# Kernel tuning notes

Measured on AMD Instinct MI355X. Metric: run time of the kernel, lower is better.

The kernel has to match this reference:

```python
import jax, jax.numpy as jnp
import numpy as np

COMMITMENT_COST = 0.25
EPS = 1e-10


def setup_inputs() -> dict:
    key = jax.random.key(0)
    k1, k2 = jax.random.split(key)
    z = jax.random.normal(k1, (8, 2048, 512), dtype=jnp.float32)
    # codebook ~ small uniform init in torch; small normal is fine for a numeric reference
    codebook = jax.random.normal(k2, (4096, 512), dtype=jnp.float32) * 0.02
    return {"z": z, "codebook": codebook}


def reference(z, codebook):
    B, S, D = z.shape
    K = codebook.shape[0]
    flat_z = z.reshape(-1, D)  # [N, D]
    distances = (
        jnp.sum(flat_z * flat_z, axis=1, keepdims=True)
        + jnp.sum(codebook * codebook, axis=1)
        - 2.0 * flat_z @ codebook.T
    )
    encoding_indices = jnp.argmin(distances, axis=1)  # [N] int
    z_q = codebook[encoding_indices].reshape(z.shape)  # gather lookup
    # commitment loss (z_q detached)
    commitment_loss = jnp.mean((z - jax.lax.stop_gradient(z_q)) ** 2)
    loss = COMMITMENT_COST * commitment_loss
    # straight-through estimator
    z_q_st = z + jax.lax.stop_gradient(z_q - z)
    # perplexity from codebook usage histogram
    N = flat_z.shape[0]
    counts = jnp.zeros((K,), dtype=jnp.float32).at[encoding_indices].add(1.0)
    avg_probs = counts / N
    perplexity = jnp.exp(-jnp.sum(avg_probs * jnp.log(avg_probs + EPS)))
    encoding_indices = encoding_indices.reshape(B, S)
    return (z_q_st, loss, encoding_indices, perplexity)
```

## Files before the change

kernel.cpp:

```cpp
#include <hip/hip_runtime.h>
#include <hip/hip_fp16.h>
#include <stdint.h>

#define B_  8
#define S_  2048
#define D_  512
#define K_  4096
#define N_  (B_ * S_)
#define NCB (K_ / 128)
#define NKB (D_ / 32)
#define MARGIN 4e-3f

typedef _Float16 half8  __attribute__((ext_vector_type(8)));
typedef float    floatx4 __attribute__((ext_vector_type(4)));

#define OFF_PV0  0
#define OFF_PI0  (OFF_PV0 + (size_t)N_ * NCB * 4)
#define OFF_PV1  (OFF_PI0 + (size_t)N_ * NCB * 4)
#define OFF_PI1  (OFF_PV1 + (size_t)N_ * NCB * 4)
#define OFF_EN   (OFF_PI1 + (size_t)N_ * NCB * 4)
#define OFF_ZN   (OFF_EN + K_ * 4)
#define OFF_CNT  (OFF_ZN + N_ * 4)
#define OFF_BL   (OFF_CNT + K_ * 4)
#define OFF_ZH   (OFF_BL + 4096 * 4)
#define OFF_EH   (OFF_ZH + (size_t)N_ * D_ * 2)

__device__ __forceinline__ bool lexlt(float va, int ia, float vb, int ib) {
    return va < vb || (va == vb && ia < ib);
}

__device__ __forceinline__ void load_lds16(const _Float16* g, _Float16* l) {
    __builtin_amdgcn_global_load_lds(
        (const __attribute__((address_space(1))) unsigned int*)(uintptr_t)g,
        (__attribute__((address_space(3))) unsigned int*)(uintptr_t)l,
        16, 0, 0);
}

__global__ __launch_bounds__(256)
void vq_prep_kernel(const float* __restrict__ z, const float* __restrict__ cb,
                    _Float16* __restrict__ zh, _Float16* __restrict__ eh,
                    float* __restrict__ znorm, float* __restrict__ enorm,
                    int* __restrict__ counts) {
    const int t = threadIdx.x;
    if (blockIdx.x < 16) counts[blockIdx.x * 256 + t] = 0;

    const size_t u = (size_t)blockIdx.x * 256 + t;
    const int c   = (int)(u & 63);
    const int row = (int)(u >> 6);
    const bool isZ = row < N_;
    const int n = isZ ? row : row - N_;
    const float* r = (isZ ? z : cb) + (size_t)n * D_;

    float s = 0.f;
    for (int j = c; j < D_; j += 64) { float v = r[j]; s += v * v; }
    #pragma unroll
    for (int m = 1; m < 64; m <<= 1) s += __shfl_xor(s, m, 64);
    if (c == 0) { if (isZ) znorm[n] = s; else enorm[n] = s; }

    const float scale = isZ ? 1.0f : 64.0f;
    const float4 v0 = *(const float4*)(r + c * 8);
    const float4 v1 = *(const float4*)(r + c * 8 + 4);
    float a[8] = {v0.x, v0.y, v0.z, v0.w, v1.x, v1.y, v1.z, v1.w};
    half8 h;
    #pragma unroll
    for (int j = 0; j < 8; j++) h[j] = (_Float16)(a[j] * scale);
    const int kb = c >> 2, qd = c & 3;
    const int sw = qd ^ ((n >> 1) & 3);
    const size_t rows = isZ ? (size_t)N_ : (size_t)K_;
    const size_t off = (size_t)kb * rows * 32 + (size_t)n * 32 + (size_t)(sw << 3);
    *(half8*)((isZ ? zh : eh) + off) = h;
}

__global__ __launch_bounds__(256, 4)
void vq_dist_kernel(const _Float16* __restrict__ zh, const _Float16* __restrict__ eh,
                    const float* __restrict__ enorm, const float* __restrict__ znorm,
                    float* __restrict__ pV0, int* __restrict__ pI0,
                    float* __restrict__ pV1, int* __restrict__ pI1) {
    __shared__ _Float16 sA[2][4096];
    __shared__ float sE[128], sZn[128];
    __shared__ float cV0[2][128], cV1[2][128];
    __shared__ int   cI0[2][128], cI1[2][128];

    const int t  = threadIdx.x;
    const int c0 = blockIdx.x * 128;
    const int m0 = blockIdx.y * 128;

    if (t < 128) { sE[t] = enorm[c0 + t]; sZn[t] = znorm[m0 + t]; }

    const int lane = t & 63, wid = t >> 6;
    const int wr = wid & 1, wc = wid >> 1;
    const int qd = lane >> 4, nl = lane & 15;
    const int sw8 = (qd ^ ((nl >> 1) & 3)) << 3;

    const _Float16* gsrc = zh + (size_t)m0 * 32 + (size_t)(wid * 2) * 512 + (size_t)lane * 8;
    const size_t strideA = (size_t)N_ * 32;
    const size_t strideB = (size_t)K_ * 32;
    const _Float16* behk = eh + (size_t)c0 * 32;

    floatx4 acc[4][4];
    #pragma unroll
    for (int i = 0; i < 4; i++)
        #pragma unroll
        for (int j = 0; j < 4; j++) acc[i][j] = (floatx4)0.f;

    #pragma unroll
    for (int g = 0; g < 2; g++)
        load_lds16(gsrc + g * 512, sA[0] + wid * 2 * 512 + g * 512);

    for (int kb = 0; kb < NKB; kb++) {
        __syncthreads();

        half8 b_h[4];
        #pragma unroll
        for (int s = 0; s < 4; s++) {
            const int br = wc * 64 + s * 16 + nl;
            b_h[s] = *(const half8*)(behk + (size_t)kb * strideB + br * 32 + sw8);
        }
        if (kb + 1 < NKB) {
            const _Float16* gk = gsrc + (size_t)(kb + 1) * strideA;
            _Float16* ld = sA[(kb + 1) & 1] + wid * 2 * 512;
            #pragma unroll
            for (int g = 0; g < 2; g++)
                load_lds16(gk + g * 512, ld + g * 512);
        }
        const _Float16* ah = sA[kb & 1];
        half8 a_h[4];
        #pragma unroll
        for (int s = 0; s < 4; s++) {
            const int ar = wr * 64 + s * 16 + nl;
            a_h[s] = *(const half8*)&ah[ar * 32 + sw8];
        }
        #pragma unroll
        for (int i = 0; i < 4; i++)
            #pragma unroll
            for (int j = 0; j < 4; j++)
                acc[i][j] = __builtin_amdgcn_mfma_f32_16x16x32_f16(a_h[i], b_h[j], acc[i][j], 0, 0, 0);
    }

    #pragma unroll
    for (int sm = 0; sm < 4; sm++) {
        #pragma unroll
        for (int reg = 0; reg < 4; reg++) {
            const int rm = wr * 64 + sm * 16 + qd * 4 + reg;
            const float zn = sZn[rm];
            float v0 = 1e30f, v1 = 1e30f; int i0 = 0x7fffffff, i1 = 0x7fffffff;
            #pragma unroll
            for (int sn = 0; sn < 4; sn++) {
                const int cl = wc * 64 + sn * 16 + nl;
                const float dot = acc[sm][sn][reg] * 0.015625f;
                const float v   = (zn + sE[cl]) - 2.0f * dot;
                const int ci = c0 + cl;
                if (lexlt(v, ci, v0, i0)) { v1 = v0; i1 = i0; v0 = v; i0 = ci; }
                else if (lexlt(v, ci, v1, i1)) { v1 = v; i1 = ci; }
            }
            #pragma unroll
            for (int msk = 1; msk <= 8; msk <<= 1) {
                const float w0 = __shfl_xor(v0, msk, 64);
                const int   j0 = __shfl_xor(i0, msk, 64);
                const float w1 = __shfl_xor(v1, msk, 64);
                const int   j1 = __shfl_xor(i1, msk, 64);
                if (lexlt(w0, j0, v0, i0)) {
                    if (lexlt(v0, i0, w1, j1)) { v1 = v0; i1 = i0; } else { v1 = w1; i1 = j1; }
                    v0 = w0; i0 = j0;
                } else if (lexlt(w0, j0, v1, i1)) { v1 = w0; i1 = j0; }
            }
            if (nl == 0) { cV0[wc][rm] = v0; cI0[wc][rm] = i0; cV1[wc][rm] = v1; cI1[wc][rm] = i1; }
        }
    }
    __syncthreads();
    if (t < 128) {
        float v0 = cV0[0][t], v1 = cV1[0][t];
        int   i0 = cI0[0][t], i1 = cI1[0][t];
        const float w0 = cV0[1][t], w1 = cV1[1][t];
        const int   j0 = cI0[1][t], j1 = cI1[1][t];
        if (lexlt(w0, j0, v0, i0)) {
            if (lexlt(v0, i0, w1, j1)) { v1 = v0; i1 = i0; } else { v1 = w1; i1 = j1; }
            v0 = w0; i0 = j0;
        } else if (lexlt(w0, j0, v1, i1)) { v1 = w0; i1 = j0; }
        const size_t o = (size_t)(m0 + t) * NCB + blockIdx.x;
        pV0[o] = v0; pI0[o] = i0; pV1[o] = v1; pI1[o] = i1;
    }
}

__global__ __launch_bounds__(256)
void vq_gather_kernel(const float* __restrict__ z, const float* __restrict__ cb,
                      const float* __restrict__ znorm, const float* __restrict__ enorm,
                      const float* __restrict__ pV0, const int* __restrict__ pI0,
                      const float* __restrict__ pV1, const int* __restrict__ pI1,
                      float* __restrict__ out_zq, float* __restrict__ out_idx,
                      int* __restrict__ counts, float* __restrict__ blockLoss) {
    const int lane = threadIdx.x & 63, wid = threadIdx.x >> 6;
    const int m = blockIdx.x * 4 + wid;

    float v0 = 1e30f, v1 = 1e30f; int i0 = 0x7fffffff, i1 = 0x7fffffff;
    if (lane < NCB) {
        const size_t o = (size_t)m * NCB + lane;
        v0 = pV0[o]; i0 = pI0[o]; v1 = pV1[o]; i1 = pI1[o];
    }
    float gv = v0; int gi = i0;
    #pragma unroll
    for (int msk = 1; msk < 64; msk <<= 1) {
        const float ov = __shfl_xor(gv, msk, 64);
        const int   oi = __shfl_xor(gi, msk, 64);
        if (lexlt(ov, oi, gv, gi)) { gv = ov; gi = oi; }
    }
    const bool f0 = (lane < NCB) && (v0 <= gv + MARGIN);
    const bool f1 = (lane < NCB) && (v1 <= gv + MARGIN);
    unsigned long long b0 = __ballot(f0), b1 = __ballot(f1);
    int idx = gi;
    if (__popcll(b0) + __popcll(b1) > 1) {
        const float zn = znorm[m];
        const float* zrow = z + (size_t)m * D_;
        float bestd = 1e30f; int besti = 0x7fffffff;
        for (int slot = 0; slot < 2; slot++) {
            unsigned long long bm = slot ? b1 : b0;
            while (bm) {
                const int l = (int)__builtin_ctzll(bm); bm &= bm - 1;
                const int cand = __shfl(slot ? i1 : i0, l, 64);
                const float* crow = cb + (size_t)cand * D_;
                float s = 0.f;
                #pragma unroll
                for (int j = 0; j < 8; j++)
                    s += zrow[lane * 8 + j] * crow[lane * 8 + j];
                #pragma unroll
                for (int msk = 1; msk < 64; msk <<= 1) s += __shfl_xor(s, msk, 64);
                const float d = (zn + enorm[cand]) - 2.0f * s;
                if (lexlt(d, cand, bestd, besti)) { bestd = d; besti = cand; }
            }
        }
        idx = besti;
    }

    const float4* qrow = (const float4*)(cb + (size_t)idx * D_);
    const float4* zrow4 = (const float4*)(z + (size_t)m * D_);
    float4*       orow = (float4*)(out_zq + (size_t)m * D_);
    float lsum = 0.f;
    #pragma unroll
    for (int i = 0; i < 2; i++) {
        const int j = lane + i * 64;
        const float4 q  = qrow[j];
        const float4 zv = zrow4[j];
        float4 o;
        o.x = zv.x + (q.x - zv.x); o.y = zv.y + (q.y - zv.y);
        o.z = zv.z + (q.z - zv.z); o.w = zv.w + (q.w - zv.w);
        orow[j] = o;
        const float dx = zv.x - q.x, dy = zv.y - q.y, dz = zv.z - q.z, dw = zv.w - q.w;
        lsum += dx * dx + dy * dy + dz * dz + dw * dw;
    }
    #pragma unroll
    for (int msk = 1; msk < 64; msk <<= 1) lsum += __shfl_xor(lsum, msk, 64);

    if (lane == 0) {
        out_idx[m] = (float)idx;
        atomicAdd(&counts[idx], 1);
    }
    __shared__ float wl[4];
    if (lane == 0) wl[wid] = lsum;
    __syncthreads();
    if (threadIdx.x == 0) blockLoss[blockIdx.x] = wl[0] + wl[1] + wl[2] + wl[3];
}

__global__ void vq_final_kernel(const int* __restrict__ counts,
                                const float* __restrict__ blockLoss,
                                float* __restrict__ out_loss, float* __restrict__ out_ppl) {
    __shared__ float sl[256], se[256];
    const int t = threadIdx.x;
    float ls = 0.f, es = 0.f;
    for (int i = t; i < N_ / 4; i += 256) ls += blockLoss[i];
    for (int k = t; k < K_; k += 256) {
        const float p = (float)counts[k] / (float)N_;
        es += p * logf(p + 1e-10f);
    }
    sl[t] = ls; se[t] = es;
    __syncthreads();
    for (int s = 128; s > 0; s >>= 1) {
        if (t < s) { sl[t] += sl[t + s]; se[t] += se[t + s]; }
        __syncthreads();
    }
    if (t == 0) {
        out_loss[0] = 0.25f * (sl[0] / (float)((size_t)N_ * D_));
        out_ppl[0]  = expf(-se[0]);
    }
}

extern "C" void kernel_launch(void* const* d_in, const int* in_sizes, int n_in,
                              void* d_out, int out_size, void* d_ws, size_t ws_size,
                              hipStream_t stream) {
    const float* z  = (const float*)d_in[0];
    const float* cb = (const float*)d_in[1];
    float* out = (float*)d_out;

    char* ws = (char*)d_ws;
    float*    pV0       = (float*)   (ws + OFF_PV0);
    int*      pI0       = (int*)     (ws + OFF_PI0);
    float*    pV1       = (float*)   (ws + OFF_PV1);
    int*      pI1       = (int*)     (ws + OFF_PI1);
    float*    enorm     = (float*)   (ws + OFF_EN);
    float*    znorm     = (float*)   (ws + OFF_ZN);
    int*      counts    = (int*)     (ws + OFF_CNT);
    float*    blockLoss = (float*)   (ws + OFF_BL);
    _Float16* zh        = (_Float16*)(ws + OFF_ZH);
    _Float16* eh        = (_Float16*)(ws + OFF_EH);

    float* out_zq   = out;
    float* out_loss = out + (size_t)N_ * D_;
    float* out_idx  = out_loss + 1;
    float* out_ppl  = out_idx + N_;

    vq_prep_kernel<<<(N_ + K_) * 64 / 256, 256, 0, stream>>>(z, cb, zh, eh,
                                                             znorm, enorm, counts);

    dim3 grid(K_ / 128, N_ / 128);
    vq_dist_kernel<<<grid, 256, 0, stream>>>(zh, eh, enorm, znorm, pV0, pI0, pV1, pI1);

    vq_gather_kernel<<<N_ / 4, 256, 0, stream>>>(z, cb, znorm, enorm,
                                                 pV0, pI0, pV1, pI1,
                                                 out_zq, out_idx, counts, blockLoss);

    vq_final_kernel<<<1, 256, 0, stream>>>(counts, blockLoss, out_loss, out_ppl);
}
```

Measured before the change: 249.8 us.

## Pack distance+index into sortable uint keys and fuse final reduction into gather

Replaces the separate value/index top-2 tracking with packed 32-bit keys: the truncated float distance in the high bits and the 7-bit local column in the low bits, reduced with unsigned min/max instead of lexicographic branches. This halves the partial-result storage and shuffle traffic. The safety margin is widened to cover the truncation error. The final loss/perplexity kernel is folded into the gather kernel through a last-block atomic counter with a polling loop, which removes one launch but adds spin risk and extra atomics. Pointer arithmetic in the MFMA loop is also hoisted.

```diff
diff --git a/kernel.cpp b/kernel.cpp
--- a/kernel.cpp
+++ b/kernel.cpp
@@ -8,23 +8,24 @@
 #define K_  4096
 #define N_  (B_ * S_)
 #define NCB (K_ / 128)
-#define NKB (D_ / 32)
-#define MARGIN 4e-3f
+#define NKB (D_ / 16)
+#define NKB32 (D_ / 32)
+#define MARGIN 0.014f
 
 typedef _Float16 half8  __attribute__((ext_vector_type(8)));
 typedef float    floatx4 __attribute__((ext_vector_type(4)));
 
-#define OFF_PV0  0
-#define OFF_PI0  (OFF_PV0 + (size_t)N_ * NCB * 4)
-#define OFF_PV1  (OFF_PI0 + (size_t)N_ * NCB * 4)
-#define OFF_PI1  (OFF_PV1 + (size_t)N_ * NCB * 4)
-#define OFF_EN   (OFF_PI1 + (size_t)N_ * NCB * 4)
+#define OFF_PK   0
+#define OFF_EN   (OFF_PK + (size_t)N_ * NCB * 8)
 #define OFF_ZN   (OFF_EN + K_ * 4)
 #define OFF_CNT  (OFF_ZN + N_ * 4)
 #define OFF_BL   (OFF_CNT + K_ * 4)
-#define OFF_ZH   (OFF_BL + 4096 * 4)
+#define OFF_DONE (OFF_BL + 4096 * 4)
+#define OFF_ZH   (OFF_DONE + 256)
 #define OFF_EH   (OFF_ZH + (size_t)N_ * D_ * 2)
 
+__device__ __forceinline__ uint32_t umin32(uint32_t a, uint32_t b) { return a < b ? a : b; }
+__device__ __forceinline__ uint32_t umax32(uint32_t a, uint32_t b) { return a > b ? a : b; }
 __device__ __forceinline__ bool lexlt(float va, int ia, float vb, int ib) {
     return va < vb || (va == vb && ia < ib);
 }
@@ -40,9 +41,12 @@
 void vq_prep_kernel(const float* __restrict__ z, const float* __restrict__ cb,
                     _Float16* __restrict__ zh, _Float16* __restrict__ eh,
                     float* __restrict__ znorm, float* __restrict__ enorm,
-                    int* __restrict__ counts) {
+                    int* __restrict__ counts, float* __restrict__ blockLoss,
+                    int* __restrict__ done) {
     const int t = threadIdx.x;
     if (blockIdx.x < 16) counts[blockIdx.x * 256 + t] = 0;
+    else if (blockIdx.x == 16 && t == 0) done[0] = 0;
+    if (blockIdx.x >= 17 && blockIdx.x < 33) blockLoss[(blockIdx.x - 17) * 256 + t] = -1.0f;
 
     const size_t u = (size_t)blockIdx.x * 256 + t;
     const int c   = (int)(u & 63);
@@ -74,12 +78,10 @@
 __global__ __launch_bounds__(256, 4)
 void vq_dist_kernel(const _Float16* __restrict__ zh, const _Float16* __restrict__ eh,
                     const float* __restrict__ enorm, const float* __restrict__ znorm,
-                    float* __restrict__ pV0, int* __restrict__ pI0,
-                    float* __restrict__ pV1, int* __restrict__ pI1) {
+                    uint2* __restrict__ pK) {
     __shared__ _Float16 sA[2][4096];
     __shared__ float sE[128], sZn[128];
-    __shared__ float cV0[2][128], cV1[2][128];
-    __shared__ int   cI0[2][128], cI1[2][128];
+    __shared__ uint2 cK[2][128];
 
     const int t  = threadIdx.x;
     const int c0 = blockIdx.x * 128;
@@ -95,7 +97,8 @@
     const _Float16* gsrc = zh + (size_t)m0 * 32 + (size_t)(wid * 2) * 512 + (size_t)lane * 8;
     const size_t strideA = (size_t)N_ * 32;
     const size_t strideB = (size_t)K_ * 32;
-    const _Float16* behk = eh + (size_t)c0 * 32;
+    const _Float16* bptr = eh + (size_t)c0 * 32 + (size_t)((wc * 64 + nl) * 32 + sw8);
+    const int aoff = (wr * 64 + nl) * 32 + sw8;
 
     floatx4 acc[4][4];
     #pragma unroll
@@ -107,116 +110,117 @@
     for (int g = 0; g < 2; g++)
         load_lds16(gsrc + g * 512, sA[0] + wid * 2 * 512 + g * 512);
 
-    for (int kb = 0; kb < NKB; kb++) {
+    for (int kb = 0; kb < NKB32; kb++) {
         __syncthreads();
 
         half8 b_h[4];
         #pragma unroll
-        for (int s = 0; s < 4; s++) {
-            const int br = wc * 64 + s * 16 + nl;
-            b_h[s] = *(const half8*)(behk + (size_t)kb * strideB + br * 32 + sw8);
-        }
-        if (kb + 1 < NKB) {
+        for (int s = 0; s < 4; s++)
+            b_h[s] = *(const half8*)(bptr + s * 512);
+        if (kb + 1 < NKB32) {
             const _Float16* gk = gsrc + (size_t)(kb + 1) * strideA;
             _Float16* ld = sA[(kb + 1) & 1] + wid * 2 * 512;
             #pragma unroll
             for (int g = 0; g < 2; g++)
                 load_lds16(gk + g * 512, ld + g * 512);
         }
-        const _Float16* ah = sA[kb & 1];
+        const _Float16* ah = sA[kb & 1] + aoff;
         half8 a_h[4];
         #pragma unroll
-        for (int s = 0; s < 4; s++) {
-            const int ar = wr * 64 + s * 16 + nl;
-            a_h[s] = *(const half8*)&ah[ar * 32 + sw8];
-        }
+        for (int s = 0; s < 4; s++)
+            a_h[s] = *(const half8*)(ah + s * 512);
         #pragma unroll
         for (int i = 0; i < 4; i++)
             #pragma unroll
             for (int j = 0; j < 4; j++)
                 acc[i][j] = __builtin_amdgcn_mfma_f32_16x16x32_f16(a_h[i], b_h[j], acc[i][j], 0, 0, 0);
-    }
-
+        bptr += strideB;
+    }
+
+    uint32_t colc[4]; float se4[4];
+    #pragma unroll
+    for (int sn = 0; sn < 4; sn++) {
+        const int cl = wc * 64 + sn * 16 + nl;
+        colc[sn] = (uint32_t)cl;
+        se4[sn]  = sE[cl];
+    }
     #pragma unroll
     for (int sm = 0; sm < 4; sm++) {
         #pragma unroll
         for (int reg = 0; reg < 4; reg++) {
             const int rm = wr * 64 + sm * 16 + qd * 4 + reg;
             const float zn = sZn[rm];
-            float v0 = 1e30f, v1 = 1e30f; int i0 = 0x7fffffff, i1 = 0x7fffffff;
+            uint32_t k0 = 0xFFFFFFFFu, k1 = 0xFFFFFFFFu;
             #pragma unroll
             for (int sn = 0; sn < 4; sn++) {
-                const int cl = wc * 64 + sn * 16 + nl;
-                const float dot = acc[sm][sn][reg] * 0.015625f;
-                const float v   = (zn + sE[cl]) - 2.0f * dot;
-                const int ci = c0 + cl;
-                if (lexlt(v, ci, v0, i0)) { v1 = v0; i1 = i0; v0 = v; i0 = ci; }
-                else if (lexlt(v, ci, v1, i1)) { v1 = v; i1 = ci; }
+                const float v = fmaf(acc[sm][sn][reg], -0.03125f, zn + se4[sn]);
+                const uint32_t key = (__float_as_uint(v) & 0xFFFFFF80u) | colc[sn];
+                const uint32_t t1 = umax32(k0, key);
+                k1 = umin32(k1, t1);
+                k0 = umin32(k0, key);
             }
             #pragma unroll
             for (int msk = 1; msk <= 8; msk <<= 1) {
-                const float w0 = __shfl_xor(v0, msk, 64);
-                const int   j0 = __shfl_xor(i0, msk, 64);
-                const float w1 = __shfl_xor(v1, msk, 64);
-                const int   j1 = __shfl_xor(i1, msk, 64);
-                if (lexlt(w0, j0, v0, i0)) {
-                    if (lexlt(v0, i0, w1, j1)) { v1 = v0; i1 = i0; } else { v1 = w1; i1 = j1; }
-                    v0 = w0; i0 = j0;
-                } else if (lexlt(w0, j0, v1, i1)) { v1 = w0; i1 = j0; }
+                const uint32_t o0 = (uint32_t)__shfl_xor((int)k0, msk, 64);
+                const uint32_t o1 = (uint32_t)__shfl_xor((int)k1, msk, 64);
+                const uint32_t n0 = umin32(k0, o0);
+                k1 = umin32(umax32(k0, o0), umin32(k1, o1));
+                k0 = n0;
             }
-            if (nl == 0) { cV0[wc][rm] = v0; cI0[wc][rm] = i0; cV1[wc][rm] = v1; cI1[wc][rm] = i1; }
+            if (nl == 0) { cK[wc][rm].x = k0; cK[wc][rm].y = k1; }
         }
     }
     __syncthreads();
     if (t < 128) {
-        float v0 = cV0[0][t], v1 = cV1[0][t];
-        int   i0 = cI0[0][t], i1 = cI1[0][t];
-        const float w0 = cV0[1][t], w1 = cV1[1][t];
-        const int   j0 = cI0[1][t], j1 = cI1[1][t];
-        if (lexlt(w0, j0, v0, i0)) {
-            if (lexlt(v0, i0, w1, j1)) { v1 = v0; i1 = i0; } else { v1 = w1; i1 = j1; }
-            v0 = w0; i0 = j0;
-        } else if (lexlt(w0, j0, v1, i1)) { v1 = w0; i1 = j0; }
-        const size_t o = (size_t)(m0 + t) * NCB + blockIdx.x;
-        pV0[o] = v0; pI0[o] = i0; pV1[o] = v1; pI1[o] = i1;
+        const uint2 a = cK[0][t], b = cK[1][t];
+        uint2 r;
+        r.x = umin32(a.x, b.x);
+        r.y = umin32(umax32(a.x, b.x), umin32(a.y, b.y));
+        pK[(size_t)(m0 + t) * NCB + blockIdx.x] = r;
     }
 }
 
 __global__ __launch_bounds__(256)
 void vq_gather_kernel(const float* __restrict__ z, const float* __restrict__ cb,
                       const float* __restrict__ znorm, const float* __restrict__ enorm,
-                      const float* __restrict__ pV0, const int* __restrict__ pI0,
-                      const float* __restrict__ pV1, const int* __restrict__ pI1,
+                      const uint2* __restrict__ pK,
                       float* __restrict__ out_zq, float* __restrict__ out_idx,
-                      int* __restrict__ counts, float* __restrict__ blockLoss) {
+                      int* __restrict__ counts, float* __restrict__ blockLoss,
+                      int* __restrict__ done,
+                      float* __restrict__ out_loss, float* __restrict__ out_ppl) {
     const int lane = threadIdx.x & 63, wid = threadIdx.x >> 6;
     const int m = blockIdx.x * 4 + wid;
 
-    float v0 = 1e30f, v1 = 1e30f; int i0 = 0x7fffffff, i1 = 0x7fffffff;
+    uint32_t k0 = 0xFFFFFFFFu, k1 = 0xFFFFFFFFu;
     if (lane < NCB) {
-        const size_t o = (size_t)m * NCB + lane;
-        v0 = pV0[o]; i0 = pI0[o]; v1 = pV1[o]; i1 = pI1[o];
-    }
-    float gv = v0; int gi = i0;
+        const uint2 kk = pK[(size_t)m * NCB + lane];
+        k0 = kk.x; k1 = kk.y;
+    }
+    uint32_t g = k0;
     #pragma unroll
     for (int msk = 1; msk < 64; msk <<= 1) {
-        const float ov = __shfl_xor(gv, msk, 64);
-        const int   oi = __shfl_xor(gi, msk, 64);
-        if (lexlt(ov, oi, gv, gi)) { gv = ov; gi = oi; }
-    }
-    const bool f0 = (lane < NCB) && (v0 <= gv + MARGIN);
-    const bool f1 = (lane < NCB) && (v1 <= gv + MARGIN);
-    unsigned long long b0 = __ballot(f0), b1 = __ballot(f1);
-    int idx = gi;
-    if (__popcll(b0) + __popcll(b1) > 1) {
+        const uint32_t o = (uint32_t)__shfl_xor((int)g, msk, 64);
+        g = umin32(g, o);
+    }
+    const float gvf = __uint_as_float(g & 0xFFFFFF80u) + MARGIN;
+    const bool f0 = (lane < NCB) && (__uint_as_float(k0 & 0xFFFFFF80u) <= gvf);
+    const bool f1 = (lane < NCB) && (__uint_as_float(k1 & 0xFFFFFF80u) <= gvf);
+    const unsigned long long b0 = __ballot(f0), b1 = __ballot(f1);
+    int idx;
+    if (__popcll(b0) + __popcll(b1) <= 1) {
+        const unsigned long long bw = __ballot(k0 == g);
+        idx = (int)__builtin_ctzll(bw) * 128 + (int)(g & 0x7Fu);
+    } else {
         const float zn = znorm[m];
         const float* zrow = z + (size_t)m * D_;
         float bestd = 1e30f; int besti = 0x7fffffff;
+        #pragma unroll
         for (int slot = 0; slot < 2; slot++) {
             unsigned long long bm = slot ? b1 : b0;
             while (bm) {
                 const int l = (int)__builtin_ctzll(bm); bm &= bm - 1;
-                const int cand = __shfl(slot ? i1 : i0, l, 64);
+                const uint32_t kx = (uint32_t)__shfl((int)(slot ? k1 : k0), l, 64);
+                const int cand = l * 128 + (int)(kx & 0x7Fu);
                 const float* crow = cb + (size_t)cand * D_;
                 float s = 0.f;
                 #pragma unroll
@@ -231,9 +235,9 @@
         idx = besti;
     }
 
-    const float4* qrow = (const float4*)(cb + (size_t)idx * D_);
+    const float4* qrow  = (const float4*)(cb + (size_t)idx * D_);
     const float4* zrow4 = (const float4*)(z + (size_t)m * D_);
-    float4*       orow = (float4*)(out_zq + (size_t)m * D_);
+    float4*       orow  = (float4*)(out_zq + (size_t)m * D_);
     float lsum = 0.f;
     #pragma unroll
     for (int i = 0; i < 2; i++) {
@@ -255,31 +259,50 @@
         atomicAdd(&counts[idx], 1);
     }
     __shared__ float wl[4];
+    __shared__ int amLast;
     if (lane == 0) wl[wid] = lsum;
     __syncthreads();
-    if (threadIdx.x == 0) blockLoss[blockIdx.x] = wl[0] + wl[1] + wl[2] + wl[3];
-}
-
-__global__ void vq_final_kernel(const int* __restrict__ counts,
-                                const float* __restrict__ blockLoss,
-                                float* __restrict__ out_loss, float* __restrict__ out_ppl) {
+    if (threadIdx.x == 0) {
+        const float bl = wl[0] + wl[1] + wl[2] + wl[3];
+        __hip_atomic_store(&blockLoss[blockIdx.x], bl, __ATOMIC_RELAXED, __HIP_MEMORY_SCOPE_AGENT);
+        const int prev = __hip_atomic_fetch_add(done, 1, __ATOMIC_RELAXED, __HIP_MEMORY_SCOPE_AGENT);
+        amLast = (prev == (int)gridDim.x - 1);
+    }
+    __syncthreads();
+    if (!amLast) return;
+
+    const int t = threadIdx.x;
     __shared__ float sl[256], se[256];
-    const int t = threadIdx.x;
-    float ls = 0.f, es = 0.f;
-    for (int i = t; i < N_ / 4; i += 256) ls += blockLoss[i];
-    for (int k = t; k < K_; k += 256) {
-        const float p = (float)counts[k] / (float)N_;
-        es += p * logf(p + 1e-10f);
-    }
-    sl[t] = ls; se[t] = es;
-    __syncthreads();
-    for (int s = 128; s > 0; s >>= 1) {
-        if (t < s) { sl[t] += sl[t + s]; se[t] += se[t + s]; }
+    __shared__ int si[256], sok[256];
+    __shared__ int goodFlag;
+    for (;;) {
+        float ls = 0.f, es = 0.f; int tot = 0, ok = 1;
+        for (int i = t; i < N_ / 4; i += 256) {
+            const float b = __hip_atomic_load(&blockLoss[i], __ATOMIC_RELAXED, __HIP_MEMORY_SCOPE_AGENT);
+            if (b >= 0.f) ls += b; else ok = 0;
+        }
+        for (int k = t; k < K_; k += 256) {
+            const int c = __hip_atomic_load(&counts[k], __ATOMIC_RELAXED, __HIP_MEMORY_SCOPE_AGENT);
+            tot += c;
+            const float p = (float)c / (float)N_;
+            es += p * logf(p + 1e-10f);
+        }
+        sl[t] = ls; se[t] = es; si[t] = tot; sok[t] = ok;
         __syncthreads();
-    }
-    if (t == 0) {
-        out_loss[0] = 0.25f * (sl[0] / (float)((size_t)N_ * D_));
-        out_ppl[0]  = expf(-se[0]);
+        for (int s = 128; s > 0; s >>= 1) {
+            if (t < s) { sl[t] += sl[t + s]; se[t] += se[t + s]; si[t] += si[t + s]; sok[t] &= sok[t + s]; }
+            __syncthreads();
+        }
+        if (t == 0) goodFlag = (si[0] == N_ && sok[0]);
+        __syncthreads();
+        if (goodFlag) {
+            if (t == 0) {
+                out_loss[0] = 0.25f * (sl[0] / (float)((size_t)N_ * D_));
+                out_ppl[0]  = expf(-se[0]);
+            }
+            return;
+        }
+        __syncthreads();
     }
 }
 
@@ -291,14 +314,12 @@
     float* out = (float*)d_out;
 
     char* ws = (char*)d_ws;
-    float*    pV0       = (float*)   (ws + OFF_PV0);
-    int*      pI0       = (int*)     (ws + OFF_PI0);
-    float*    pV1       = (float*)   (ws + OFF_PV1);
-    int*      pI1       = (int*)     (ws + OFF_PI1);
+    uint2*    pK        = (uint2*)   (ws + OFF_PK);
     float*    enorm     = (float*)   (ws + OFF_EN);
     float*    znorm     = (float*)   (ws + OFF_ZN);
     int*      counts    = (int*)     (ws + OFF_CNT);
     float*    blockLoss = (float*)   (ws + OFF_BL);
+    int*      done      = (int*)     (ws + OFF_DONE);
     _Float16* zh        = (_Float16*)(ws + OFF_ZH);
     _Float16* eh        = (_Float16*)(ws + OFF_EH);
 
@@ -308,14 +329,13 @@
     float* out_ppl  = out_idx + N_;
 
     vq_prep_kernel<<<(N_ + K_) * 64 / 256, 256, 0, stream>>>(z, cb, zh, eh,
-                                                             znorm, enorm, counts);
+                                                             znorm, enorm, counts,
+                                                             blockLoss, done);
 
     dim3 grid(K_ / 128, N_ / 128);
-    vq_dist_kernel<<<grid, 256, 0, stream>>>(zh, eh, enorm, znorm, pV0, pI0, pV1, pI1);
-
-    vq_gather_kernel<<<N_ / 4, 256, 0, stream>>>(z, cb, znorm, enorm,
-                                                 pV0, pI0, pV1, pI1,
-                                                 out_zq, out_idx, counts, blockLoss);
-
-    vq_final_kernel<<<1, 256, 0, stream>>>(counts, blockLoss, out_loss, out_ppl);
-}
+    vq_dist_kernel<<<grid, 256, 0, stream>>>(zh, eh, enorm, znorm, pK);
+
+    vq_gather_kernel<<<N_ / 4, 256, 0, stream>>>(z, cb, znorm, enorm, pK,
+                                                 out_zq, out_idx, counts, blockLoss,
+                                                 done, out_loss, out_ppl);
+}
```

Result: faster. 244.0 us (-2.3%).
